# Performance work log

Measured on AMD Instinct MI355X. Metric: run time of the kernel, lower is better.

## Reference

```python
import jax, jax.numpy as jnp
import numpy as np

BINS = 32  # position_bins


def setup_inputs() -> dict:
    key = jax.random.key(0)
    ks = jax.random.split(key, 7)
    N, IN, E = 1024, 21, 128
    return {
        "target_feat": jax.random.normal(ks[0], (N, IN), dtype=jnp.float32),
        "residue_index": jnp.arange(N, dtype=jnp.int64),
        "Wa": jax.random.normal(ks[1], (E, IN), dtype=jnp.float32) * 0.1,
        "ba": jax.random.normal(ks[2], (E,), dtype=jnp.float32) * 0.1,
        "Wb": jax.random.normal(ks[3], (E, IN), dtype=jnp.float32) * 0.1,
        "bb": jax.random.normal(ks[4], (E,), dtype=jnp.float32) * 0.1,
        "Wp": jax.random.normal(ks[5], (E, 2 * BINS + 1), dtype=jnp.float32) * 0.1,
        "bp": jax.random.normal(ks[6], (E,), dtype=jnp.float32) * 0.1,
    }


def reference(target_feat, residue_index, Wa, ba, Wb, bb, Wp, bp):
    # Linear projections: [N, E]
    a = target_feat @ Wa.T + ba
    b = target_feat @ Wb.T + bb
    # Relative position bucket: [N, N] int in [0, 2*BINS]
    d = residue_index[:, None] - residue_index[None, :]
    d = jnp.clip(d, -BINS, BINS) + BINS
    # one_hot(d) @ Wp.T + bp  ==  row gather from Wp.T (fused, no one-hot)
    p = jnp.take(Wp.T, d, axis=0) + bp  # [N, N, E]
    # Outer broadcast sum z = a_i + b_j plus position term
    return a[:, None, :] + b[None, :, :] + p
```

## Files before the change

kernel.cpp:

```cpp
#include <hip/hip_runtime.h>

#define NN    1024
#define INF   21
#define EE    128
#define NB    65
#define BINSV 32

typedef float f32x4 __attribute__((ext_vector_type(4)));

__global__ __launch_bounds__(128) void prep_kernel(
    const float* __restrict__ tf,
    const float* __restrict__ Wa, const float* __restrict__ ba,
    const float* __restrict__ Wb, const float* __restrict__ bb,
    const float* __restrict__ Wp, const float* __restrict__ bp,
    float* __restrict__ a, float* __restrict__ b, float* __restrict__ ptab) {
  const int e = threadIdx.x;
  if (blockIdx.x < NN) {
    const int i = blockIdx.x;
    __shared__ float row[INF];
    if (e < INF) row[e] = tf[i * INF + e];
    __syncthreads();
    float sa = ba[e];
    float sb = bb[e];
#pragma unroll
    for (int k = 0; k < INF; ++k) {
      float r = row[k];
      sa = fmaf(r, Wa[e * INF + k], sa);
      sb = fmaf(r, Wb[e * INF + k], sb);
    }
    a[i * EE + e] = sa;
    b[i * EE + e] = sb;
  } else {
    const int d = blockIdx.x - NN;
    ptab[d * EE + e] = Wp[e * NB + d] + bp[e];
  }
}

__global__ __launch_bounds__(512) void fill_kernel(
    const float* __restrict__ a, const float* __restrict__ b,
    const float* __restrict__ ptab, const int* __restrict__ ri,
    float* __restrict__ out) {
  __shared__ int sri[NN];
  const int tid = threadIdx.x;
  for (int t = tid; t < NN; t += 512) sri[t] = ri[t];
  __syncthreads();

  const int lane = tid & 63;
  const int hi   = lane >> 5;
  const int e4   = lane & 31;
  const int w    = blockIdx.x * 8 + (tid >> 6);
  const int jp   = w & 511;
  const int ic   = w >> 9;
  const int j    = 2 * jp + hi;

  const f32x4* __restrict__ a4 = reinterpret_cast<const f32x4*>(a);
  const f32x4* __restrict__ p4 = reinterpret_cast<const f32x4*>(ptab);

  const f32x4 bv = reinterpret_cast<const f32x4*>(b + j * EE)[e4];
  const int rj = sri[j];

  f32x4* __restrict__ o4 = reinterpret_cast<f32x4*>(out);

#pragma unroll 4
  for (int t = 0; t < 64; ++t) {
    const int i = t * 16 + ic;
    const f32x4 av = a4[i * 32 + e4];
    int d = sri[i] - rj;
    d = min(max(d, -BINSV), BINSV) + BINSV;
    const f32x4 pv = p4[d * 32 + e4];
    const f32x4 o = av + bv + pv;
    const size_t u = (size_t)t * 8192 + w;
    __builtin_nontemporal_store(o, o4 + u * 64 + hi * 32 + e4);
  }
}

extern "C" void kernel_launch(void* const* d_in, const int* in_sizes, int n_in,
                              void* d_out, int out_size, void* d_ws, size_t ws_size,
                              hipStream_t stream) {
  const float* tf = (const float*)d_in[0];
  const int*   ri = (const int*)d_in[1];
  const float* Wa = (const float*)d_in[2];
  const float* ba = (const float*)d_in[3];
  const float* Wb = (const float*)d_in[4];
  const float* bb = (const float*)d_in[5];
  const float* Wp = (const float*)d_in[6];
  const float* bp = (const float*)d_in[7];
  float* out = (float*)d_out;

  float* ws   = (float*)d_ws;
  float* a    = ws;
  float* b    = ws + NN * EE;
  float* ptab = ws + 2 * NN * EE;

  prep_kernel<<<NN + NB, 128, 0, stream>>>(tf, Wa, ba, Wb, bb, Wp, bp, a, b, ptab);
  fill_kernel<<<NN, 512, 0, stream>>>(a, b, ptab, ri, out);
}
```

Baseline: 110.8 us.

## Tile fill kernel into 32x32 (i,j) blocks with register-reused b rows

Replaces the 1D wave mapping with a 2D grid of 32x32 output tiles. Each wave holds four b rows and their residue indices in registers and loops over 32 i rows, reusing each loaded a row across four outputs. Blocks shrink to 256 threads with an occupancy hint of 8 blocks per CU. The goal is fewer redundant loads of a and b and more concurrent blocks, at the cost of a different store locality pattern for a kernel that is bound by output writes.

```diff
diff --git a/kernel.cpp b/kernel.cpp
--- a/kernel.cpp
+++ b/kernel.cpp
@@ -5,6 +5,8 @@
 #define EE    128
 #define NB    65
 #define BINSV 32
+#define TI    32
+#define TJ    32
 
 typedef float f32x4 __attribute__((ext_vector_type(4)));
 
@@ -36,41 +38,50 @@
   }
 }
 
-__global__ __launch_bounds__(512) void fill_kernel(
+__global__ __launch_bounds__(256, 8) void fill_kernel(
     const float* __restrict__ a, const float* __restrict__ b,
     const float* __restrict__ ptab, const int* __restrict__ ri,
     float* __restrict__ out) {
   __shared__ int sri[NN];
   const int tid = threadIdx.x;
-  for (int t = tid; t < NN; t += 512) sri[t] = ri[t];
+  for (int t = tid; t < NN; t += 256) sri[t] = ri[t];
   __syncthreads();
 
   const int lane = tid & 63;
   const int hi   = lane >> 5;
   const int e4   = lane & 31;
-  const int w    = blockIdx.x * 8 + (tid >> 6);
-  const int jp   = w & 511;
-  const int ic   = w >> 9;
-  const int j    = 2 * jp + hi;
+  const int wv   = tid >> 6;
+  const int i0   = blockIdx.y * TI;
+  const int j0   = blockIdx.x * TJ;
 
   const f32x4* __restrict__ a4 = reinterpret_cast<const f32x4*>(a);
+  const f32x4* __restrict__ b4 = reinterpret_cast<const f32x4*>(b);
   const f32x4* __restrict__ p4 = reinterpret_cast<const f32x4*>(ptab);
 
-  const f32x4 bv = reinterpret_cast<const f32x4*>(b + j * EE)[e4];
-  const int rj = sri[j];
+  int   jr[4];
+  f32x4 bv[4];
+  int   rj[4];
+#pragma unroll
+  for (int jj = 0; jj < 4; ++jj) {
+    jr[jj] = j0 + jj * 8 + wv * 2 + hi;
+    bv[jj] = b4[jr[jj] * 32 + e4];
+    rj[jj] = sri[jr[jj]];
+  }
 
   f32x4* __restrict__ o4 = reinterpret_cast<f32x4*>(out);
 
-#pragma unroll 4
-  for (int t = 0; t < 64; ++t) {
-    const int i = t * 16 + ic;
+  for (int ii = 0; ii < TI; ++ii) {
+    const int i = i0 + ii;
     const f32x4 av = a4[i * 32 + e4];
-    int d = sri[i] - rj;
-    d = min(max(d, -BINSV), BINSV) + BINSV;
-    const f32x4 pv = p4[d * 32 + e4];
-    const f32x4 o = av + bv + pv;
-    const size_t u = (size_t)t * 8192 + w;
-    __builtin_nontemporal_store(o, o4 + u * 64 + hi * 32 + e4);
+    const int rii = sri[i];
+    const size_t orow = (size_t)i * NN;
+#pragma unroll
+    for (int jj = 0; jj < 4; ++jj) {
+      int d = rii - rj[jj];
+      d = min(max(d, -BINSV), BINSV) + BINSV;
+      const f32x4 o = av + bv[jj] + p4[d * 32 + e4];
+      __builtin_nontemporal_store(o, o4 + (orow + jr[jj]) * 32 + e4);
+    }
   }
 }
 
@@ -93,5 +104,6 @@
   float* ptab = ws + 2 * NN * EE;
 
   prep_kernel<<<NN + NB, 128, 0, stream>>>(tf, Wa, ba, Wb, bb, Wp, bp, a, b, ptab);
-  fill_kernel<<<NN, 512, 0, stream>>>(a, b, ptab, ri, out);
+  dim3 grid(NN / TJ, NN / TI);
+  fill_kernel<<<grid, 256, 0, stream>>>(a, b, ptab, ri, out);
 }
```

After: 127.5 us. 15.0% more time.
